# Optimization experiments

Measured on AMD Instinct MI355X. Metric: run time of the kernel, lower is better.

The kernel has to match this reference:

```python
import jax, jax.numpy as jnp
from jax import lax
import numpy as np

B, N, C, P = 8, 512, 256, 7
CQ = C // 4
NMS_THRESH = 0.5
BBOX_XFORM_CLIP = 4.135166556742356  # log(1000/16)


def setup_inputs():
    key = jax.random.key(0)
    ks = jax.random.split(key, 24)
    rn = lambda k, s, sc=0.02: jax.random.normal(k, s, jnp.float32) * sc
    box_feats_q = jax.random.normal(ks[0], (B, N, C, P, P), jnp.float32)
    box_feats_s = jax.random.normal(ks[1], (B, 1, C, P, P), jnp.float32)
    xy = jax.random.uniform(ks[2], (B, N, 2), jnp.float32, 0.0, 700.0)
    wh = jax.random.uniform(ks[3], (B, N, 2), jnp.float32, 8.0, 96.0)
    proposals = jnp.concatenate([xy, xy + wh], axis=-1)  # [B,N,4] valid x1y1x2y2
    image_size = jnp.array([800, 800], jnp.int32)  # (H, W)
    return {
        'box_feats_q': box_feats_q, 'box_feats_s': box_feats_s,
        'proposals': proposals, 'image_size': image_size,
        'W1': rn(ks[4], (CQ, 2 * C)),          # conv1 1x1: 2C -> C/4
        'W2': rn(ks[5], (CQ, CQ, 3, 3)),       # conv2 3x3 valid
        'W3': rn(ks[6], (C, CQ)),              # conv3 1x1: C/4 -> C
        'Wcor': rn(ks[7], (C, C)),             # conv_cor 1x1
        'fc1_w': rn(ks[8], (C, 2 * C)), 'fc1_b': jnp.zeros((C,), jnp.float32),
        'fc2_w': rn(ks[9], (C, C)), 'fc2_b': jnp.zeros((C,), jnp.float32),
        'sfc_w': rn(ks[10], (1, C)), 'sfc_b': jnp.zeros((1,), jnp.float32),
        'scor_w': rn(ks[11], (1, C)), 'scor_b': jnp.zeros((1,), jnp.float32),
        'spr_w': rn(ks[12], (1, C)), 'spr_b': jnp.zeros((1,), jnp.float32),
        'dpr_w': rn(ks[13], (4, C)), 'dpr_b': jnp.zeros((4,), jnp.float32),
    }


def avgpool3(x):  # AvgPool2d(3, stride=1), NCHW
    s = lax.reduce_window(x, 0.0, lax.add, (1, 1, 3, 3), (1, 1, 1, 1), 'VALID')
    return s / 9.0


def head_forward(box_feats_q, box_feats_s, W1, W2, W3, Wcor, fc1_w, fc1_b, fc2_w,
                 fc2_b, sfc_w, sfc_b, scor_w, scor_b, spr_w, spr_b, dpr_w, dpr_b):
    M = B * N
    x_q = box_feats_q.reshape(M, C, P, P)
    x_s = jnp.broadcast_to(box_feats_s, (B, N, C, P, P)).reshape(M, C, P, P)
    # FC branch (avgpool_fc == global mean over 7x7)
    x_fc = jnp.concatenate([x_q.mean((2, 3)), x_s.mean((2, 3))], axis=1)  # [M,2C]
    h = jax.nn.relu(x_fc @ fc1_w.T + fc1_b)
    h = jax.nn.relu(h @ fc2_w.T + fc2_b)
    score_fc = h @ sfc_w.T + sfc_b  # [M,1]
    # Correlation branch: grouped 7x7 conv == per-channel spatial dot product
    x_cor_q = jnp.einsum('oc,mchw->mohw', Wcor, x_q)
    x_cor_s = jnp.einsum('oc,mchw->mohw', Wcor, x_s)
    x_relu = jax.nn.relu((x_cor_q * x_cor_s).sum((2, 3)))  # [M,C]
    score_cor = x_relu @ scor_w.T + scor_b  # [M,1]
    # Conv branch
    x = jnp.concatenate([x_q, x_s], axis=1)                    # [M,2C,7,7]
    x = jax.nn.relu(jnp.einsum('oc,mchw->mohw', W1, x))        # [M,CQ,7,7]
    x = avgpool3(x)                                            # [M,CQ,5,5]
    x = jax.nn.relu(lax.conv_general_dilated(x, W2, (1, 1), 'VALID',
        dimension_numbers=('NCHW', 'OIHW', 'NCHW')))           # [M,CQ,3,3]
    x = jax.nn.relu(jnp.einsum('oc,mchw->mohw', W3, x))        # [M,C,3,3]
    x = avgpool3(x).squeeze(3).squeeze(2)                      # [M,C]
    score_pr = x @ spr_w.T + spr_b
    pred_scores = score_pr + score_cor + score_fc              # [M,1]
    pred_deltas = x @ dpr_w.T + dpr_b                          # [M,4]
    return pred_scores, pred_deltas


def decode_boxes(deltas, boxes):
    w = boxes[:, 2] - boxes[:, 0]
    h = boxes[:, 3] - boxes[:, 1]
    cx = boxes[:, 0] + 0.5 * w
    cy = boxes[:, 1] + 0.5 * h
    dx, dy = deltas[:, 0], deltas[:, 1]
    dw = jnp.minimum(deltas[:, 2], BBOX_XFORM_CLIP)
    dh = jnp.minimum(deltas[:, 3], BBOX_XFORM_CLIP)
    pcx, pcy = dx * w + cx, dy * h + cy
    pw, ph = jnp.exp(dw) * w, jnp.exp(dh) * h
    return jnp.stack([pcx - 0.5 * pw, pcy - 0.5 * ph,
                      pcx + 0.5 * pw, pcy + 0.5 * ph], axis=1)


def nms_mask(boxes, scores, thresh):  # fixed-shape NMS -> keep mask [n]
    n = boxes.shape[0]
    order = jnp.argsort(-scores)
    b = boxes[order]
    area = jnp.maximum(b[:, 2] - b[:, 0], 0) * jnp.maximum(b[:, 3] - b[:, 1], 0)
    idx = jnp.arange(n)

    def body(i, keep):
        x1 = jnp.maximum(b[i, 0], b[:, 0]); y1 = jnp.maximum(b[i, 1], b[:, 1])
        x2 = jnp.minimum(b[i, 2], b[:, 2]); y2 = jnp.minimum(b[i, 3], b[:, 3])
        inter = jnp.maximum(x2 - x1, 0) * jnp.maximum(y2 - y1, 0)
        iou = inter / jnp.maximum(area[i] + area - inter, 1e-9)
        suppress = (iou > thresh) & (idx > i) & keep[i]
        return keep & ~suppress

    keep_sorted = lax.fori_loop(0, n, body, jnp.ones((n,), bool))
    return jnp.zeros((n,), bool).at[order].set(keep_sorted)


def reference(box_feats_q, box_feats_s, proposals, image_size, W1, W2, W3, Wcor,
              fc1_w, fc1_b, fc2_w, fc2_b, sfc_w, sfc_b, scor_w, scor_b,
              spr_w, spr_b, dpr_w, dpr_b):
    pred_scores, pred_deltas = head_forward(
        box_feats_q, box_feats_s, W1, W2, W3, Wcor, fc1_w, fc1_b, fc2_w, fc2_b,
        sfc_w, sfc_b, scor_w, scor_b, spr_w, spr_b, dpr_w, dpr_b)
    M = B * N
    # decode on detached deltas
    pred_boxes = decode_boxes(lax.stop_gradient(pred_deltas), proposals.reshape(M, 4))
    H = image_size[0].astype(jnp.float32)
    W_ = image_size[1].astype(jnp.float32)
    pred_boxes = jnp.stack([
        jnp.clip(pred_boxes[:, 0], 0.0, W_), jnp.clip(pred_boxes[:, 1], 0.0, H),
        jnp.clip(pred_boxes[:, 2], 0.0, W_), jnp.clip(pred_boxes[:, 3], 0.0, H)],
        axis=1).reshape(B, N, 4)
    scores = jax.nn.sigmoid(lax.stop_gradient(pred_scores)).reshape(B, N)
    keep = jax.vmap(lambda bx, sc: nms_mask(bx, sc, NMS_THRESH))(pred_boxes, scores)
    # boxes/scores padded to fixed [B,N,...]; keep mask marks NMS survivors
    return pred_boxes, scores, keep
```

## Files before the change

### kernel.cpp

```cpp
#include <hip/hip_runtime.h>
#include <math.h>

typedef float f4 __attribute__((ext_vector_type(4)));
typedef f4 f4u __attribute__((aligned(4)));
typedef float f32x4 __attribute__((ext_vector_type(4)));
typedef short short8 __attribute__((ext_vector_type(8)));

constexpr int NB  = 8;
constexpr int NN  = 512;
constexpr int NC  = 256;
constexpr int NHW = 49;
constexpr int NM  = NB * NN;
constexpr int XS  = 260;

constexpr size_t WS_SMEAN = 0;
constexpr size_t WS_YST   = 2048;
constexpr size_t WS_UST   = 102400;
constexpr size_t WS_WFH   = 127488;
constexpr size_t WS_WFL   = 168448;
constexpr size_t WS_SP    = 209408;
constexpr size_t WS_QMEAN = 213504;
constexpr size_t WS_SBOX  = WS_QMEAN;
constexpr size_t WS_SAREA = WS_SBOX + 16384;
constexpr size_t WS_SIDX  = WS_SAREA + 4096;
constexpr size_t WS_MASK  = WS_SIDX + 4096;

constexpr size_t OUT_SCORES = (size_t)NM * 4;
constexpr size_t OUT_KEEP   = OUT_SCORES + NM;

__device__ __forceinline__ unsigned short bf16_rne(float f) {
    unsigned u = __float_as_uint(f);
    return (unsigned short)((u + 0x7FFFu + ((u >> 16) & 1u)) >> 16);
}
__device__ __forceinline__ float bf16_to_f(unsigned short h) {
    return __uint_as_float(((unsigned)h) << 16);
}

__device__ __forceinline__ void stage_xT(const float* __restrict__ g, float* sx, int t) {
#pragma unroll
    for (int rep = 0; rep < 13; ++rep) {
        int id = rep * 256 + t;
        if (id < 3136) {
            int c4 = id / 49;
            int hw = id - c4 * 49;
            f4 v;
            v[0] = g[(c4 * 4 + 0) * 49 + hw];
            v[1] = g[(c4 * 4 + 1) * 49 + hw];
            v[2] = g[(c4 * 4 + 2) * 49 + hw];
            v[3] = g[(c4 * 4 + 3) * 49 + hw];
            *(f4*)&sx[hw * XS + c4 * 4] = v;
        }
    }
}

__global__ __launch_bounds__(256, 2) void k_prep(
    const float* __restrict__ bfs, const float* __restrict__ Wcor,
    const float* __restrict__ W1, float* __restrict__ ws)
{
    int t = threadIdx.x, blk = blockIdx.x;

    if (blk >= 64) {
        int ob = (blk - 64) * 4 + (t >> 6);
        int l = t & 63;
        int mt = ob >> 3, ks = ob & 7;
        int row = mt * 16 + (l & 15);
        int k0 = ks * 32 + (l >> 4) * 8;
        const float* src = (row < 256) ? (Wcor + (size_t)row * 256 + k0)
                                       : (W1 + (size_t)(row - 256) * 512 + k0);
        short hv[8], lv[8];
#pragma unroll
        for (int j = 0; j < 8; ++j) {
            float v = src[j];
            unsigned short hh = bf16_rne(v);
            unsigned short hl = bf16_rne(v - bf16_to_f(hh));
            hv[j] = (short)hh; lv[j] = (short)hl;
        }
        short* dh = (short*)(ws + WS_WFH) + ((size_t)ob * 64 + l) * 8;
        short* dl = (short*)(ws + WS_WFL) + ((size_t)ob * 64 + l) * 8;
#pragma unroll
        for (int j = 0; j < 8; ++j) { dh[j] = hv[j]; dl[j] = lv[j]; }
        return;
    }

    __shared__ __align__(16) float smem[49 * XS + 16];
    float* sx = smem;
    int b = blk >> 3;
    int og8 = blk & 7;

    stage_xT(bfs + (size_t)b * 12544, sx, t);
    __syncthreads();

    if (og8 == 0) {
        float s = 0.f;
        for (int hw = 0; hw < 49; ++hw) s += sx[hw * XS + t];
        ws[WS_SMEAN + (size_t)b * 256 + t] = s * (1.f / 49.f);
    }

    int og2 = t >> 3, hwg = t & 7;
    int hwb = (hwg == 7) ? 0 : hwg * 7;
    int oA = og8 * 32 + og2;
    bool do_u = (og8 < 2);
    int o2 = og8 * 32 + og2;

    float acc0[7] = {0,0,0,0,0,0,0};
    float a1a[7]  = {0,0,0,0,0,0,0};
    const float* xrow = sx + hwb * XS;
    const float* w0r = Wcor + (size_t)oA * 256;
    const float* war = W1 + (size_t)o2 * 512 + 256;

#pragma unroll 1
    for (int c4 = 0; c4 < 64; ++c4) {
        f4 xv[7];
#pragma unroll
        for (int i = 0; i < 7; ++i) xv[i] = *(const f4*)&xrow[i * XS + c4 * 4];
        f4 w0 = *(const f4*)&w0r[c4 * 4];
        f4 wa = *(const f4*)&war[c4 * 4];
#pragma unroll
        for (int j = 0; j < 4; ++j) {
#pragma unroll
            for (int i = 0; i < 7; ++i) {
                float x = xv[i][j];
                acc0[i] = fmaf(w0[j], x, acc0[i]);
                a1a[i]  = fmaf(wa[j], x, a1a[i]);
            }
        }
    }

    if (hwg < 7) {
#pragma unroll
        for (int i = 0; i < 7; ++i) {
            int hw = hwb + i;
            ws[WS_YST + ((size_t)b * 256 + oA) * 49 + hw] = acc0[i];
            if (do_u)
                ws[WS_UST + ((size_t)b * 64 + o2) * 49 + hw] = a1a[i];
        }
    }
}

__global__ __launch_bounds__(256, 3) void k_heavy(
    const float* __restrict__ bfq,
    const float* __restrict__ W2, const float* __restrict__ W3,
    const float* __restrict__ scor_w, const float* __restrict__ scor_b,
    const float* __restrict__ spr_w, const float* __restrict__ spr_b,
    const float* __restrict__ dpr_w, const float* __restrict__ dpr_b,
    const float* __restrict__ proposals, const int* __restrict__ image_size,
    float* __restrict__ ws, float* __restrict__ out)
{
    __shared__ __align__(16) short xh[49 * 256];
    __shared__ __align__(16) short xl[49 * 256];
    __shared__ float red[20];

    int t = threadIdx.x, m = blockIdx.x, b = m >> 9;
    const float* xg = bfq + (size_t)m * 12544 + (size_t)t * 49;

    {
        float qs = 0.f;
#pragma unroll
        for (int r = 0; r < 12; ++r) {
            f4u v = *(const f4u*)&xg[r * 4];
#pragma unroll
            for (int j = 0; j < 4; ++j) {
                int hw = r * 4 + j;
                float x = v[j];
                qs += x;
                unsigned short hh = bf16_rne(x);
                int idx = (hw * 256 + t) ^ ((hw & 7) << 3);
                xh[idx] = (short)hh;
                xl[idx] = (short)bf16_rne(x - bf16_to_f(hh));
            }
        }
        float x48 = xg[48];
        qs += x48;
        unsigned short hh48 = bf16_rne(x48);
        xh[48 * 256 + t] = (short)hh48;
        xl[48 * 256 + t] = (short)bf16_rne(x48 - bf16_to_f(hh48));
        ws[WS_QMEAN + (size_t)m * 256 + t] = qs * (1.f / 49.f);
    }
    __syncthreads();

    int w = t >> 6, l = t & 63, cl = l & 15, g = l >> 4;

    f32x4 acc[5][4];
#pragma unroll
    for (int i = 0; i < 5; ++i)
#pragma unroll
        for (int nt = 0; nt < 4; ++nt) acc[i][nt] = (f32x4)0.f;

    const short* wfH = (const short*)(ws + WS_WFH);
    const short* wfL = (const short*)(ws + WS_WFL);

    int bcol[4];
#pragma unroll
    for (int nt = 0; nt < 4; ++nt) {
        int col = nt * 16 + cl;
        if (col >= 49) col = 0;
        bcol[nt] = col;
    }

#pragma unroll 1
    for (int ks = 0; ks < 8; ++ks) {
        short8 bh[4], bl[4];
#pragma unroll
        for (int nt = 0; nt < 4; ++nt) {
            int col = bcol[nt];
            int idx = (col * 256 + ks * 32 + g * 8) ^ ((col & 7) << 3);
            bh[nt] = *(const short8*)&xh[idx];
            bl[nt] = *(const short8*)&xl[idx];
        }
#pragma unroll
        for (int i = 0; i < 5; ++i) {
            int mt = w + 4 * i;
            size_t off = ((size_t)(mt * 8 + ks) * 64 + l) * 8;
            short8 ah = *(const short8*)&wfH[off];
            short8 al = *(const short8*)&wfL[off];
            acc[i][0] = __builtin_amdgcn_mfma_f32_16x16x32_bf16(ah, bh[0], acc[i][0], 0, 0, 0);
            acc[i][1] = __builtin_amdgcn_mfma_f32_16x16x32_bf16(ah, bh[1], acc[i][1], 0, 0, 0);
            acc[i][2] = __builtin_amdgcn_mfma_f32_16x16x32_bf16(ah, bh[2], acc[i][2], 0, 0, 0);
            acc[i][3] = __builtin_amdgcn_mfma_f32_16x16x32_bf16(ah, bh[3], acc[i][3], 0, 0, 0);
            acc[i][0] = __builtin_amdgcn_mfma_f32_16x16x32_bf16(ah, bl[0], acc[i][0], 0, 0, 0);
            acc[i][1] = __builtin_amdgcn_mfma_f32_16x16x32_bf16(ah, bl[1], acc[i][1], 0, 0, 0);
            acc[i][2] = __builtin_amdgcn_mfma_f32_16x16x32_bf16(ah, bl[2], acc[i][2], 0, 0, 0);
            acc[i][3] = __builtin_amdgcn_mfma_f32_16x16x32_bf16(ah, bl[3], acc[i][3], 0, 0, 0);
            acc[i][0] = __builtin_amdgcn_mfma_f32_16x16x32_bf16(al, bh[0], acc[i][0], 0, 0, 0);
            acc[i][1] = __builtin_amdgcn_mfma_f32_16x16x32_bf16(al, bh[1], acc[i][1], 0, 0, 0);
            acc[i][2] = __builtin_amdgcn_mfma_f32_16x16x32_bf16(al, bh[2], acc[i][2], 0, 0, 0);
            acc[i][3] = __builtin_amdgcn_mfma_f32_16x16x32_bf16(al, bh[3], acc[i][3], 0, 0, 0);
        }
    }

    float csum = 0.f;
    {
        const float* yb = ws + WS_YST + (size_t)b * 256 * 49;
#pragma unroll
        for (int i = 0; i < 4; ++i) {
            int row0 = (w + 4 * i) * 16 + g * 4;
#pragma unroll
            for (int q = 0; q < 4; ++q) {
                int row = row0 + q;
                float p = 0.f;
#pragma unroll
                for (int nt = 0; nt < 4; ++nt) {
                    int col = nt * 16 + cl;
                    if (col < 49) p += acc[i][nt][q] * yb[(size_t)row * 49 + col];
                }
                p += __shfl_xor(p, 1, 64);
                p += __shfl_xor(p, 2, 64);
                p += __shfl_xor(p, 4, 64);
                p += __shfl_xor(p, 8, 64);
                if (cl == 0) csum += fmaxf(p, 0.f) * scor_w[row];
            }
        }
    }
    __syncthreads();

    float* s1    = (float*)xh;
    float* sp1   = s1 + 64 * 52;
    float* cpart = (float*)xl;
    float* sc2T  = cpart + 2816;
    {
        const float* ub = ws + WS_UST + (size_t)b * 64 * 49;
        int ch0 = w * 16 + g * 4;
#pragma unroll
        for (int q = 0; q < 4; ++q) {
            int ch = ch0 + q;
#pragma unroll
            for (int nt = 0; nt < 4; ++nt) {
                int col = nt * 16 + cl;
                if (col < 49)
                    s1[ch * 52 + col] = fmaxf(acc[4][nt][q] + ub[(size_t)ch * 49 + col], 0.f);
            }
        }
    }
    __syncthreads();

    for (int i = t; i < 64 * 25; i += 256) {
        int ch = i / 25, pos = i - ch * 25;
        int py = pos / 5, px = pos - py * 5;
        const float* base = s1 + ch * 52 + py * 7 + px;
        float s = base[0] + base[1] + base[2]
                + base[7] + base[8] + base[9]
                + base[14] + base[15] + base[16];
        sp1[ch * 28 + pos] = s * (1.f / 9.f);
    }
    __syncthreads();

    {
        int oc = t & 63, icq = t >> 6;
        float a9[9] = {0,0,0,0,0,0,0,0,0};
        const float* wb2 = W2 + (size_t)oc * 576 + icq * 16 * 9;
#pragma unroll 1
        for (int ic16 = 0; ic16 < 16; ++ic16) {
            int ic = icq * 16 + ic16;
            const f4* ar = (const f4*)(sp1 + ic * 28);
            float av[28];
            *(f4*)&av[0]  = ar[0];
            *(f4*)&av[4]  = ar[1];
            *(f4*)&av[8]  = ar[2];
            *(f4*)&av[12] = ar[3];
            *(f4*)&av[16] = ar[4];
            *(f4*)&av[20] = ar[5];
            *(f4*)&av[24] = ar[6];
            const float* wi = wb2 + ic16 * 9;
            f4u w0 = *(const f4u*)wi;
            f4u w1 = *(const f4u*)(wi + 4);
            float wv[9] = { w0[0], w0[1], w0[2], w0[3], w1[0], w1[1], w1[2], w1[3], wi[8] };
#pragma unroll
            for (int py = 0; py < 3; ++py)
#pragma unroll
                for (int px = 0; px < 3; ++px) {
                    int p9 = py * 3 + px;
#pragma unroll
                    for (int ky = 0; ky < 3; ++ky)
#pragma unroll
                        for (int kx = 0; kx < 3; ++kx)
                            a9[p9] = fmaf(wv[ky * 3 + kx],
                                          av[(py + ky) * 5 + (px + kx)], a9[p9]);
                }
        }
#pragma unroll
        for (int p = 0; p < 9; ++p)
            cpart[((size_t)icq * 64 + oc) * 11 + p] = a9[p];
    }
    __syncthreads();

    for (int i = t; i < 576; i += 256) {
        int pos = i >> 6, occ = i & 63;
        float s = cpart[((size_t)0 * 64 + occ) * 11 + pos]
                + cpart[((size_t)1 * 64 + occ) * 11 + pos]
                + cpart[((size_t)2 * 64 + occ) * 11 + pos]
                + cpart[((size_t)3 * 64 + occ) * 11 + pos];
        sc2T[pos * 64 + occ] = fmaxf(s, 0.f);
    }
    __syncthreads();

    float xfin;
    {
        float xw[9] = {0,0,0,0,0,0,0,0,0};
        const f4* wr = (const f4*)(W3 + (size_t)t * 64);
#pragma unroll 1
        for (int gg = 0; gg < 16; ++gg) {
            f4 wv4 = wr[gg];
#pragma unroll
            for (int p = 0; p < 9; ++p) {
                f4 c = *(const f4*)(sc2T + p * 64 + gg * 4);
                xw[p] = fmaf(wv4[0], c[0], xw[p]);
                xw[p] = fmaf(wv4[1], c[1], xw[p]);
                xw[p] = fmaf(wv4[2], c[2], xw[p]);
                xw[p] = fmaf(wv4[3], c[3], xw[p]);
            }
        }
        float s = 0.f;
#pragma unroll
        for (int p = 0; p < 9; ++p) s += fmaxf(xw[p], 0.f);
        xfin = s * (1.f / 9.f);
    }

    float v0 = xfin * spr_w[t] + csum;
    float v1 = xfin * dpr_w[0 * 256 + t];
    float v2 = xfin * dpr_w[1 * 256 + t];
    float v3 = xfin * dpr_w[2 * 256 + t];
    float v4 = xfin * dpr_w[3 * 256 + t];
#pragma unroll
    for (int off = 32; off > 0; off >>= 1) {
        v0 += __shfl_xor(v0, off, 64);
        v1 += __shfl_xor(v1, off, 64);
        v2 += __shfl_xor(v2, off, 64);
        v3 += __shfl_xor(v3, off, 64);
        v4 += __shfl_xor(v4, off, 64);
    }
    if (l == 0) {
        red[w * 5 + 0] = v0; red[w * 5 + 1] = v1; red[w * 5 + 2] = v2;
        red[w * 5 + 3] = v3; red[w * 5 + 4] = v4;
    }
    __syncthreads();

    if (t == 0) {
        float r_s  = red[0] + red[5] + red[10] + red[15];
        float r_d0 = red[1] + red[6] + red[11] + red[16];
        float r_d1 = red[2] + red[7] + red[12] + red[17];
        float r_d2 = red[3] + red[8] + red[13] + red[18];
        float r_d3 = red[4] + red[9] + red[14] + red[19];

        ws[WS_SP + m] = r_s + spr_b[0] + scor_b[0];

        float d0 = r_d0 + dpr_b[0];
        float d1 = r_d1 + dpr_b[1];
        float d2 = fminf(r_d2 + dpr_b[2], 4.135166556742356f);
        float d3 = fminf(r_d3 + dpr_b[3], 4.135166556742356f);

        const float* pr = proposals + (size_t)m * 4;
        float x1p = pr[0], y1p = pr[1], x2p = pr[2], y2p = pr[3];
        float wd = x2p - x1p, hd = y2p - y1p;
        float cx = x1p + 0.5f * wd, cy = y1p + 0.5f * hd;
        float pcx = d0 * wd + cx, pcy = d1 * hd + cy;
        float pw = expf(d2) * wd, ph = expf(d3) * hd;
        float Wf = (float)image_size[1];
        float Hf = (float)image_size[0];
        out[(size_t)m * 4 + 0] = fminf(fmaxf(pcx - 0.5f * pw, 0.f), Wf);
        out[(size_t)m * 4 + 1] = fminf(fmaxf(pcy - 0.5f * ph, 0.f), Hf);
        out[(size_t)m * 4 + 2] = fminf(fmaxf(pcx + 0.5f * pw, 0.f), Wf);
        out[(size_t)m * 4 + 3] = fminf(fmaxf(pcy + 0.5f * ph, 0.f), Hf);
    }
}

__global__ __launch_bounds__(256) void k_fc(
    const float* __restrict__ fc1_w, const float* __restrict__ fc1_b,
    const float* __restrict__ fc2_w, const float* __restrict__ fc2_b,
    const float* __restrict__ sfc_w, const float* __restrict__ sfc_b,
    float* __restrict__ ws, float* __restrict__ out)
{
    __shared__ __align__(16) float sxfc[16][512];
    __shared__ __align__(16) float sh1[16][256];
    __shared__ float s_red[64];
    int t = threadIdx.x;
    int m0 = blockIdx.x * 16;
    int w = t >> 6, l = t & 63;

#pragma unroll
    for (int mi = 0; mi < 16; ++mi) {
        int mg = m0 + mi;
        int b = mg >> 9;
        sxfc[mi][t]       = ws[WS_QMEAN + (size_t)mg * 256 + t];
        sxfc[mi][256 + t] = ws[WS_SMEAN + (size_t)b * 256 + t];
    }
    __syncthreads();

    {
        const f4* wr = (const f4*)(fc1_w + t * 512);
        float acc[16];
#pragma unroll
        for (int mi = 0; mi < 16; ++mi) acc[mi] = 0.f;
#pragma unroll 1
        for (int k4 = 0; k4 < 128; ++k4) {
            f4 wv = wr[k4];
#pragma unroll
            for (int mi = 0; mi < 16; ++mi) {
                f4 x = ((const f4*)sxfc[mi])[k4];
                acc[mi] = fmaf(wv[0], x[0], acc[mi]);
                acc[mi] = fmaf(wv[1], x[1], acc[mi]);
                acc[mi] = fmaf(wv[2], x[2], acc[mi]);
                acc[mi] = fmaf(wv[3], x[3], acc[mi]);
            }
        }
        float bb = fc1_b[t];
#pragma unroll
        for (int mi = 0; mi < 16; ++mi) sh1[mi][t] = fmaxf(acc[mi] + bb, 0.f);
    }
    __syncthreads();

    float val[16];
    {
        const f4* wr = (const f4*)(fc2_w + t * 256);
        float acc[16];
#pragma unroll
        for (int mi = 0; mi < 16; ++mi) acc[mi] = 0.f;
#pragma unroll 1
        for (int k4 = 0; k4 < 64; ++k4) {
            f4 wv = wr[k4];
#pragma unroll
            for (int mi = 0; mi < 16; ++mi) {
                f4 x = ((const f4*)sh1[mi])[k4];
                acc[mi] = fmaf(wv[0], x[0], acc[mi]);
                acc[mi] = fmaf(wv[1], x[1], acc[mi]);
                acc[mi] = fmaf(wv[2], x[2], acc[mi]);
                acc[mi] = fmaf(wv[3], x[3], acc[mi]);
            }
        }
        float bb = fc2_b[t];
        float sw = sfc_w[t];
#pragma unroll
        for (int mi = 0; mi < 16; ++mi) val[mi] = sw * fmaxf(acc[mi] + bb, 0.f);
    }

#pragma unroll
    for (int mi = 0; mi < 16; ++mi) {
        float v = val[mi];
#pragma unroll
        for (int off = 32; off > 0; off >>= 1) v += __shfl_xor(v, off, 64);
        if (l == 0) s_red[w * 16 + mi] = v;
    }
    __syncthreads();

    if (t < 16) {
        float r = s_red[0 * 16 + t] + s_red[1 * 16 + t]
                + s_red[2 * 16 + t] + s_red[3 * 16 + t];
        float tot = ws[WS_SP + m0 + t] + (r + sfc_b[0]);
        out[OUT_SCORES + m0 + t] = 1.0f / (1.0f + expf(-tot));
    }
}

__global__ __launch_bounds__(256) void k_sort(
    const float* __restrict__ out, float* __restrict__ ws)
{
    __shared__ float ssc[512];
    int t = threadIdx.x, b = blockIdx.x;
    const float* sc_g = out + OUT_SCORES + (size_t)b * 512;
    ssc[t] = sc_g[t];
    ssc[t + 256] = sc_g[t + 256];
    __syncthreads();

#pragma unroll
    for (int ii = 0; ii < 2; ++ii) {
        int i = t + ii * 256;
        float si = ssc[i];
        int r = 0;
        for (int j = 0; j < 512; ++j) {
            float sj = ssc[j];
            r += (int)((sj > si) || (sj == si && j < i));
        }
        f4 v = *(const f4*)(out + ((size_t)b * 512 + i) * 4);
        *(f4*)&ws[WS_SBOX + ((size_t)b * 512 + r) * 4] = v;
        ws[WS_SAREA + (size_t)b * 512 + r] =
            fmaxf(v[2] - v[0], 0.f) * fmaxf(v[3] - v[1], 0.f);
        ((int*)ws)[WS_SIDX + (size_t)b * 512 + r] = i;
    }
}

__global__ __launch_bounds__(256) void k_mask(float* __restrict__ ws)
{
    int t = threadIdx.x;
    int wv = t >> 6, lane = t & 63;
    int gi = blockIdx.x * 4 + wv;
    int b = gi >> 9, i = gi & 511;

    f4 bi = *(const f4*)&ws[WS_SBOX + ((size_t)b * 512 + i) * 4];
    float ai = ws[WS_SAREA + (size_t)b * 512 + i];
    unsigned long long* mask = (unsigned long long*)(ws + WS_MASK);

#pragma unroll
    for (int w = 0; w < 8; ++w) {
        int j = w * 64 + lane;
        f4 bj = *(const f4*)&ws[WS_SBOX + ((size_t)b * 512 + j) * 4];
        float aj = ws[WS_SAREA + (size_t)b * 512 + j];
        float xx1 = fmaxf(bi[0], bj[0]), yy1 = fmaxf(bi[1], bj[1]);
        float xx2 = fminf(bi[2], bj[2]), yy2 = fminf(bi[3], bj[3]);
        float inter = fmaxf(xx2 - xx1, 0.f) * fmaxf(yy2 - yy1, 0.f);
        float iou = inter / fmaxf(ai + aj - inter, 1e-9f);
        bool sup = (iou > 0.5f) && (j > i);
        unsigned long long bal = __ballot(sup);
        if (lane == 0) mask[((size_t)b * 512 + i) * 8 + w] = bal;
    }
}

__global__ __launch_bounds__(64) void k_final(
    float* __restrict__ out, const float* __restrict__ wsf)
{
    int lane = threadIdx.x, b = blockIdx.x;
    const unsigned long long* mask =
        (const unsigned long long*)(wsf + WS_MASK) + (size_t)b * 512 * 8;

    unsigned long long kw = ~0ull;
    unsigned long long nxt = (lane < 8) ? mask[lane] : 0ull;

    for (int i = 0; i < 512; ++i) {
        unsigned long long cur = nxt;
        if (i < 511 && lane < 8) nxt = mask[(size_t)(i + 1) * 8 + lane];
        unsigned long long wi = __shfl(kw, i >> 6, 64);
        if ((wi >> (i & 63)) & 1ull) {
            if (lane < 8) kw &= ~cur;
        }
    }

    const int* sidx = ((const int*)wsf) + WS_SIDX + (size_t)b * 512;
#pragma unroll
    for (int w = 0; w < 8; ++w) {
        unsigned long long word = __shfl(kw, w, 64);
        int r = w * 64 + lane;
        out[OUT_KEEP + (size_t)b * 512 + sidx[r]] =
            ((word >> lane) & 1ull) ? 1.0f : 0.0f;
    }
}

extern "C" void kernel_launch(void* const* d_in, const int* in_sizes, int n_in,
                              void* d_out, int out_size, void* d_ws, size_t ws_size,
                              hipStream_t stream) {
    const float* bfq       = (const float*)d_in[0];
    const float* bfs       = (const float*)d_in[1];
    const float* proposals = (const float*)d_in[2];
    const int*   image_sz  = (const int*)d_in[3];
    const float* W1        = (const float*)d_in[4];
    const float* W2        = (const float*)d_in[5];
    const float* W3        = (const float*)d_in[6];
    const float* Wcor      = (const float*)d_in[7];
    const float* fc1_w     = (const float*)d_in[8];
    const float* fc1_b     = (const float*)d_in[9];
    const float* fc2_w     = (const float*)d_in[10];
    const float* fc2_b     = (const float*)d_in[11];
    const float* sfc_w     = (const float*)d_in[12];
    const float* sfc_b     = (const float*)d_in[13];
    const float* scor_w    = (const float*)d_in[14];
    const float* scor_b    = (const float*)d_in[15];
    const float* spr_w     = (const float*)d_in[16];
    const float* spr_b     = (const float*)d_in[17];
    const float* dpr_w     = (const float*)d_in[18];
    const float* dpr_b     = (const float*)d_in[19];
    float* out = (float*)d_out;
    float* ws  = (float*)d_ws;

    k_prep<<<104, 256, 0, stream>>>(bfs, Wcor, W1, ws);
    k_heavy<<<NM, 256, 0, stream>>>(bfq, W2, W3,
                                    scor_w, scor_b, spr_w, spr_b,
                                    dpr_w, dpr_b, proposals, image_sz, ws, out);
    k_fc<<<NM / 16, 256, 0, stream>>>(fc1_w, fc1_b, fc2_w, fc2_b,
                                      sfc_w, sfc_b, ws, out);
    k_sort<<<NB, 256, 0, stream>>>(out, ws);
    k_mask<<<1024, 256, 0, stream>>>(ws);
    k_final<<<NB, 64, 0, stream>>>(out, ws);
}
```

Before: 494.6 us.

## Run 3x3 conv via split-bf16 MFMA and fuse NMS into one kernel

The per-thread scalar 3x3 conv in k_heavy is replaced, when the workspace is large enough, by an im2col staged into shared memory as hi/lo bf16 pairs, then 16x16x32 bf16 MFMAs with three-term split precision against W2, which k_prep pre-packs. Separately, the sort, mask and final NMS kernels are merged into one 1024-thread block per image that keeps boxes and masks in shared memory, removing two launches and global round-trips. The MFMA path depends on ws_size at runtime and gives up a little precision compared with fp32. The fused NMS runs only 8 blocks.

```diff
diff --git a/kernel.cpp b/kernel.cpp
--- a/kernel.cpp
+++ b/kernel.cpp
@@ -20,13 +20,22 @@
 constexpr size_t WS_WFL   = 168448;
 constexpr size_t WS_SP    = 209408;
 constexpr size_t WS_QMEAN = 213504;
-constexpr size_t WS_SBOX  = WS_QMEAN;
-constexpr size_t WS_SAREA = WS_SBOX + 16384;
-constexpr size_t WS_SIDX  = WS_SAREA + 4096;
-constexpr size_t WS_MASK  = WS_SIDX + 4096;
+constexpr size_t WS_W2FH  = 1262080;
+constexpr size_t WS_W2FL  = 1280512;
+constexpr size_t WS_NEED_BIG = 1298944;
 
 constexpr size_t OUT_SCORES = (size_t)NM * 4;
 constexpr size_t OUT_KEEP   = OUT_SCORES + NM;
+
+__device__ __forceinline__ float block_reduce_sum(float v, float* red) {
+    int t = threadIdx.x;
+#pragma unroll
+    for (int off = 32; off > 0; off >>= 1) v += __shfl_down(v, off, 64);
+    __syncthreads();
+    if ((t & 63) == 0) red[t >> 6] = v;
+    __syncthreads();
+    return red[0] + red[1] + red[2] + red[3];
+}
 
 __device__ __forceinline__ unsigned short bf16_rne(float f) {
     unsigned u = __float_as_uint(f);
@@ -55,9 +64,29 @@
 
 __global__ __launch_bounds__(256, 2) void k_prep(
     const float* __restrict__ bfs, const float* __restrict__ Wcor,
-    const float* __restrict__ W1, float* __restrict__ ws)
+    const float* __restrict__ W1, const float* __restrict__ W2,
+    float* __restrict__ ws, int use_mfma_conv)
 {
     int t = threadIdx.x, blk = blockIdx.x;
+
+    if (blk >= 104) {
+        if (!use_mfma_conv) return;
+        int ks2 = blk - 104;
+        int mt = t >> 6, l = t & 63;
+        int row = mt * 16 + (l & 15);
+        int kk0 = ks2 * 32 + (l >> 4) * 8;
+        const float* src = W2 + (size_t)row * 576 + kk0;
+        short* dh = (short*)(ws + WS_W2FH) + ((size_t)(mt * 18 + ks2) * 64 + l) * 8;
+        short* dl = (short*)(ws + WS_W2FL) + ((size_t)(mt * 18 + ks2) * 64 + l) * 8;
+#pragma unroll
+        for (int j = 0; j < 8; ++j) {
+            float v = src[j];
+            unsigned short hh = bf16_rne(v);
+            dh[j] = (short)hh;
+            dl[j] = (short)bf16_rne(v - bf16_to_f(hh));
+        }
+        return;
+    }
 
     if (blk >= 64) {
         int ob = (blk - 64) * 4 + (t >> 6);
@@ -144,7 +173,7 @@
     const float* __restrict__ spr_w, const float* __restrict__ spr_b,
     const float* __restrict__ dpr_w, const float* __restrict__ dpr_b,
     const float* __restrict__ proposals, const int* __restrict__ image_size,
-    float* __restrict__ ws, float* __restrict__ out)
+    float* __restrict__ ws, float* __restrict__ out, int use_mfma_conv)
 {
     __shared__ __align__(16) short xh[49 * 256];
     __shared__ __align__(16) short xl[49 * 256];
@@ -255,8 +284,9 @@
 
     float* s1    = (float*)xh;
     float* sp1   = s1 + 64 * 52;
+    float* sc2T  = s1 + 5120;
     float* cpart = (float*)xl;
-    float* sc2T  = cpart + 2816;
+
     {
         const float* ub = ws + WS_UST + (size_t)b * 64 * 49;
         int ch0 = w * 16 + g * 4;
@@ -284,54 +314,101 @@
     }
     __syncthreads();
 
-    {
-        int oc = t & 63, icq = t >> 6;
-        float a9[9] = {0,0,0,0,0,0,0,0,0};
-        const float* wb2 = W2 + (size_t)oc * 576 + icq * 16 * 9;
-#pragma unroll 1
-        for (int ic16 = 0; ic16 < 16; ++ic16) {
-            int ic = icq * 16 + ic16;
-            const f4* ar = (const f4*)(sp1 + ic * 28);
-            float av[28];
-            *(f4*)&av[0]  = ar[0];
-            *(f4*)&av[4]  = ar[1];
-            *(f4*)&av[8]  = ar[2];
-            *(f4*)&av[12] = ar[3];
-            *(f4*)&av[16] = ar[4];
-            *(f4*)&av[20] = ar[5];
-            *(f4*)&av[24] = ar[6];
-            const float* wi = wb2 + ic16 * 9;
-            f4u w0 = *(const f4u*)wi;
-            f4u w1 = *(const f4u*)(wi + 4);
-            float wv[9] = { w0[0], w0[1], w0[2], w0[3], w1[0], w1[1], w1[2], w1[3], wi[8] };
+    if (use_mfma_conv) {
+        short* bimh = (short*)xl;
+        short* biml = ((short*)xl) + 5184;
+#pragma unroll 1
+        for (int kk = t; kk < 576; kk += 256) {
+            int ic = kk / 9;
+            int k  = kk - ic * 9;
+            int ky = k / 3, kx = k - ky * 3;
+            const float* bsp = sp1 + ic * 28 + ky * 5 + kx;
 #pragma unroll
             for (int py = 0; py < 3; ++py)
 #pragma unroll
                 for (int px = 0; px < 3; ++px) {
-                    int p9 = py * 3 + px;
-#pragma unroll
-                    for (int ky = 0; ky < 3; ++ky)
-#pragma unroll
-                        for (int kx = 0; kx < 3; ++kx)
-                            a9[p9] = fmaf(wv[ky * 3 + kx],
-                                          av[(py + ky) * 5 + (px + kx)], a9[p9]);
+                    int pos = py * 3 + px;
+                    float v = bsp[py * 5 + px];
+                    unsigned short hh = bf16_rne(v);
+                    int idx = pos * 576 + (kk ^ ((pos & 7) << 3));
+                    bimh[idx] = (short)hh;
+                    biml[idx] = (short)bf16_rne(v - bf16_to_f(hh));
                 }
         }
-#pragma unroll
-        for (int p = 0; p < 9; ++p)
-            cpart[((size_t)icq * 64 + oc) * 11 + p] = a9[p];
-    }
-    __syncthreads();
-
-    for (int i = t; i < 576; i += 256) {
-        int pos = i >> 6, occ = i & 63;
-        float s = cpart[((size_t)0 * 64 + occ) * 11 + pos]
-                + cpart[((size_t)1 * 64 + occ) * 11 + pos]
-                + cpart[((size_t)2 * 64 + occ) * 11 + pos]
-                + cpart[((size_t)3 * 64 + occ) * 11 + pos];
-        sc2T[pos * 64 + occ] = fmaxf(s, 0.f);
-    }
-    __syncthreads();
+        __syncthreads();
+
+        f32x4 a2 = (f32x4)0.f;
+        const short* w2h = (const short*)(ws + WS_W2FH);
+        const short* w2l = (const short*)(ws + WS_W2FL);
+        int c9 = (cl < 9) ? cl : 0;
+        int bbase = c9 * 576, bxor = (c9 & 7) << 3;
+#pragma unroll 1
+        for (int ks2 = 0; ks2 < 18; ++ks2) {
+            int bidx = bbase + ((ks2 * 32 + g * 8) ^ bxor);
+            short8 bh = *(const short8*)&bimh[bidx];
+            short8 bl = *(const short8*)&biml[bidx];
+            size_t off = ((size_t)(w * 18 + ks2) * 64 + l) * 8;
+            short8 ah = *(const short8*)&w2h[off];
+            short8 al = *(const short8*)&w2l[off];
+            a2 = __builtin_amdgcn_mfma_f32_16x16x32_bf16(ah, bh, a2, 0, 0, 0);
+            a2 = __builtin_amdgcn_mfma_f32_16x16x32_bf16(ah, bl, a2, 0, 0, 0);
+            a2 = __builtin_amdgcn_mfma_f32_16x16x32_bf16(al, bh, a2, 0, 0, 0);
+        }
+        if (cl < 9) {
+#pragma unroll
+            for (int q = 0; q < 4; ++q)
+                sc2T[cl * 64 + (w * 16 + g * 4 + q)] = fmaxf(a2[q], 0.f);
+        }
+        __syncthreads();
+    } else {
+        {
+            int oc = t & 63, icq = t >> 6;
+            float a9[9] = {0,0,0,0,0,0,0,0,0};
+            const float* wb2 = W2 + (size_t)oc * 576 + icq * 16 * 9;
+#pragma unroll 1
+            for (int ic16 = 0; ic16 < 16; ++ic16) {
+                int ic = icq * 16 + ic16;
+                const f4* ar = (const f4*)(sp1 + ic * 28);
+                float av[28];
+                *(f4*)&av[0]  = ar[0];
+                *(f4*)&av[4]  = ar[1];
+                *(f4*)&av[8]  = ar[2];
+                *(f4*)&av[12] = ar[3];
+                *(f4*)&av[16] = ar[4];
+                *(f4*)&av[20] = ar[5];
+                *(f4*)&av[24] = ar[6];
+                const float* wi = wb2 + ic16 * 9;
+                f4u w0 = *(const f4u*)wi;
+                f4u w1 = *(const f4u*)(wi + 4);
+                float wv[9] = { w0[0], w0[1], w0[2], w0[3], w1[0], w1[1], w1[2], w1[3], wi[8] };
+#pragma unroll
+                for (int py = 0; py < 3; ++py)
+#pragma unroll
+                    for (int px = 0; px < 3; ++px) {
+                        int p9 = py * 3 + px;
+#pragma unroll
+                        for (int ky = 0; ky < 3; ++ky)
+#pragma unroll
+                            for (int kx = 0; kx < 3; ++kx)
+                                a9[p9] = fmaf(wv[ky * 3 + kx],
+                                              av[(py + ky) * 5 + (px + kx)], a9[p9]);
+                    }
+            }
+#pragma unroll
+            for (int p = 0; p < 9; ++p)
+                cpart[((size_t)(t >> 6) * 64 + (t & 63)) * 11 + p] = a9[p];
+        }
+        __syncthreads();
+        for (int i = t; i < 576; i += 256) {
+            int pos = i >> 6, occ = i & 63;
+            float s = cpart[((size_t)0 * 64 + occ) * 11 + pos]
+                    + cpart[((size_t)1 * 64 + occ) * 11 + pos]
+                    + cpart[((size_t)2 * 64 + occ) * 11 + pos]
+                    + cpart[((size_t)3 * 64 + occ) * 11 + pos];
+            sc2T[pos * 64 + occ] = fmaxf(s, 0.f);
+        }
+        __syncthreads();
+    }
 
     float xfin;
     {
@@ -489,85 +566,75 @@
     }
 }
 
-__global__ __launch_bounds__(256) void k_sort(
-    const float* __restrict__ out, float* __restrict__ ws)
+__global__ __launch_bounds__(1024) void k_nms(float* __restrict__ out)
 {
     __shared__ float ssc[512];
+    __shared__ __align__(16) float sbox[512 * 4];
+    __shared__ float sarea[512];
+    __shared__ int   sidx[512];
+    __shared__ unsigned long long smask[512 * 8];
+
     int t = threadIdx.x, b = blockIdx.x;
+    int wv = t >> 6, lane = t & 63;
     const float* sc_g = out + OUT_SCORES + (size_t)b * 512;
-    ssc[t] = sc_g[t];
-    ssc[t + 256] = sc_g[t + 256];
-    __syncthreads();
-
-#pragma unroll
-    for (int ii = 0; ii < 2; ++ii) {
-        int i = t + ii * 256;
-        float si = ssc[i];
+
+    if (t < 512) ssc[t] = sc_g[t];
+    __syncthreads();
+
+    if (t < 512) {
+        float si = ssc[t];
         int r = 0;
         for (int j = 0; j < 512; ++j) {
             float sj = ssc[j];
-            r += (int)((sj > si) || (sj == si && j < i));
-        }
-        f4 v = *(const f4*)(out + ((size_t)b * 512 + i) * 4);
-        *(f4*)&ws[WS_SBOX + ((size_t)b * 512 + r) * 4] = v;
-        ws[WS_SAREA + (size_t)b * 512 + r] =
-            fmaxf(v[2] - v[0], 0.f) * fmaxf(v[3] - v[1], 0.f);
-        ((int*)ws)[WS_SIDX + (size_t)b * 512 + r] = i;
-    }
-}
-
-__global__ __launch_bounds__(256) void k_mask(float* __restrict__ ws)
-{
-    int t = threadIdx.x;
-    int wv = t >> 6, lane = t & 63;
-    int gi = blockIdx.x * 4 + wv;
-    int b = gi >> 9, i = gi & 511;
-
-    f4 bi = *(const f4*)&ws[WS_SBOX + ((size_t)b * 512 + i) * 4];
-    float ai = ws[WS_SAREA + (size_t)b * 512 + i];
-    unsigned long long* mask = (unsigned long long*)(ws + WS_MASK);
-
-#pragma unroll
-    for (int w = 0; w < 8; ++w) {
-        int j = w * 64 + lane;
-        f4 bj = *(const f4*)&ws[WS_SBOX + ((size_t)b * 512 + j) * 4];
-        float aj = ws[WS_SAREA + (size_t)b * 512 + j];
-        float xx1 = fmaxf(bi[0], bj[0]), yy1 = fmaxf(bi[1], bj[1]);
-        float xx2 = fminf(bi[2], bj[2]), yy2 = fminf(bi[3], bj[3]);
-        float inter = fmaxf(xx2 - xx1, 0.f) * fmaxf(yy2 - yy1, 0.f);
-        float iou = inter / fmaxf(ai + aj - inter, 1e-9f);
-        bool sup = (iou > 0.5f) && (j > i);
-        unsigned long long bal = __ballot(sup);
-        if (lane == 0) mask[((size_t)b * 512 + i) * 8 + w] = bal;
-    }
-}
-
-__global__ __launch_bounds__(64) void k_final(
-    float* __restrict__ out, const float* __restrict__ wsf)
-{
-    int lane = threadIdx.x, b = blockIdx.x;
-    const unsigned long long* mask =
-        (const unsigned long long*)(wsf + WS_MASK) + (size_t)b * 512 * 8;
-
-    unsigned long long kw = ~0ull;
-    unsigned long long nxt = (lane < 8) ? mask[lane] : 0ull;
-
-    for (int i = 0; i < 512; ++i) {
-        unsigned long long cur = nxt;
-        if (i < 511 && lane < 8) nxt = mask[(size_t)(i + 1) * 8 + lane];
-        unsigned long long wi = __shfl(kw, i >> 6, 64);
-        if ((wi >> (i & 63)) & 1ull) {
-            if (lane < 8) kw &= ~cur;
-        }
-    }
-
-    const int* sidx = ((const int*)wsf) + WS_SIDX + (size_t)b * 512;
-#pragma unroll
-    for (int w = 0; w < 8; ++w) {
-        unsigned long long word = __shfl(kw, w, 64);
-        int r = w * 64 + lane;
-        out[OUT_KEEP + (size_t)b * 512 + sidx[r]] =
-            ((word >> lane) & 1ull) ? 1.0f : 0.0f;
+            r += (int)((sj > si) || (sj == si && j < t));
+        }
+        f4 v = *(const f4*)(out + ((size_t)b * 512 + t) * 4);
+        *(f4*)&sbox[r * 4] = v;
+        sarea[r] = fmaxf(v[2] - v[0], 0.f) * fmaxf(v[3] - v[1], 0.f);
+        sidx[r] = t;
+    }
+    __syncthreads();
+
+#pragma unroll 1
+    for (int k = 0; k < 32; ++k) {
+        int i = wv * 32 + k;
+        f4 bi = *(const f4*)&sbox[i * 4];
+        float ai = sarea[i];
+#pragma unroll
+        for (int w8 = 0; w8 < 8; ++w8) {
+            int j = w8 * 64 + lane;
+            f4 bj = *(const f4*)&sbox[j * 4];
+            float aj = sarea[j];
+            float xx1 = fmaxf(bi[0], bj[0]), yy1 = fmaxf(bi[1], bj[1]);
+            float xx2 = fminf(bi[2], bj[2]), yy2 = fminf(bi[3], bj[3]);
+            float inter = fmaxf(xx2 - xx1, 0.f) * fmaxf(yy2 - yy1, 0.f);
+            float iou = inter / fmaxf(ai + aj - inter, 1e-9f);
+            bool sup = (iou > 0.5f) && (j > i);
+            unsigned long long bal = __ballot(sup);
+            if (lane == 0) smask[i * 8 + w8] = bal;
+        }
+    }
+    __syncthreads();
+
+    if (wv == 0) {
+        unsigned long long kw = ~0ull;
+        unsigned long long nxt = (lane < 8) ? smask[lane] : 0ull;
+        for (int i = 0; i < 512; ++i) {
+            unsigned long long cur = nxt;
+            if (i < 511 && lane < 8) nxt = smask[(size_t)(i + 1) * 8 + lane];
+            unsigned long long wi = __shfl(kw, i >> 6, 64);
+            if ((wi >> (i & 63)) & 1ull) {
+                if (lane < 8) kw &= ~cur;
+            }
+        }
+        if (lane < 8) smask[lane] = kw;
+    }
+    __syncthreads();
+
+    if (t < 512) {
+        unsigned long long word = smask[t >> 6];
+        out[OUT_KEEP + (size_t)b * 512 + sidx[t]] =
+            ((word >> (t & 63)) & 1ull) ? 1.0f : 0.0f;
     }
 }
 
@@ -597,13 +664,13 @@
     float* out = (float*)d_out;
     float* ws  = (float*)d_ws;
 
-    k_prep<<<104, 256, 0, stream>>>(bfs, Wcor, W1, ws);
+    int big = (ws_size >= WS_NEED_BIG * sizeof(float)) ? 1 : 0;
+
+    k_prep<<<big ? 122 : 104, 256, 0, stream>>>(bfs, Wcor, W1, W2, ws, big);
     k_heavy<<<NM, 256, 0, stream>>>(bfq, W2, W3,
                                     scor_w, scor_b, spr_w, spr_b,
-                                    dpr_w, dpr_b, proposals, image_sz, ws, out);
+                                    dpr_w, dpr_b, proposals, image_sz, ws, out, big);
     k_fc<<<NM / 16, 256, 0, stream>>>(fc1_w, fc1_b, fc2_w, fc2_b,
                                       sfc_w, sfc_b, ws, out);
-    k_sort<<<NB, 256, 0, stream>>>(out, ws);
-    k_mask<<<1024, 256, 0, stream>>>(ws);
-    k_final<<<NB, 64, 0, stream>>>(out, ws);
-}
+    k_nms<<<NB, 1024, 0, stream>>>(out);
+}
```

Result: faster. 448.1 us (-9.4%).
